# Optimization experiments

Measured on AMD Instinct MI355X. Metric: run time of the kernel, lower is better.

## Reference

```python
import jax, jax.numpy as jnp
import numpy as np

B, N, D, K = 8, 200000, 16, 512
MAX_CP = K  # upper bound on number of condensation points per event
ATTR_W, REPL_W, BG_W = 1.0, 1.0, 2.0


def setup_inputs() -> dict:
    key = jax.random.key(0)
    k1, k2, k3 = jax.random.split(key, 3)
    beta = jax.random.normal(k1, (B, N, 1), jnp.float32)
    embed = jax.random.normal(k2, (B, N, D), jnp.float32)
    r = jax.random.randint(k3, (B, N), 0, K + 8)
    slice_id = jnp.where(r < K, r, -1).astype(jnp.int32)

    def _first_occ(sid_b):
        fg = sid_b >= 0
        seg = jnp.where(fg, sid_b, K)
        fi = jax.ops.segment_min(jnp.where(fg, jnp.arange(N), N), seg, num_segments=K + 1)[:K]
        present = fi < N
        return jnp.clip(fi, 0, N - 1), present

    fi, pres = jax.vmap(_first_occ)(slice_id)
    # exactly one condensation point per present instance (its first hit)
    is_cp = jnp.zeros((B, N), jnp.int32).at[jnp.arange(B)[:, None], fi].max(pres.astype(jnp.int32))
    return {"beta": beta, "embed": embed, "slice_id": slice_id, "is_cp": is_cp}


def _per_event(beta_b, emb_b, sid, cp):
    # beta_b:[N], emb_b:[N,D], sid:[N] int, cp:[N] int
    fg = sid >= 0
    bg = ~fg
    seg = jnp.where(fg, sid, K)            # background -> dummy segment K
    sid_c = jnp.clip(sid, 0, K - 1)
    counts = jax.ops.segment_sum(fg.astype(jnp.float32), seg, num_segments=K + 1)[:K]
    present = counts > 0
    cp_fg = (cp == 1) & fg
    cp_cnt = jax.ops.segment_sum(cp_fg.astype(jnp.float32), seg, num_segments=K + 1)[:K]
    valid = present & (cp_cnt == 1)        # instances entering the CE term

    # per-instance cross-entropy: lse(beta over instance hits) - beta[cp]
    beta_m = jnp.where(fg, beta_b, -jnp.inf)
    m = jax.ops.segment_max(beta_m, seg, num_segments=K + 1)[:K]
    m_safe = jnp.where(jnp.isfinite(m), m, 0.0)
    e = jnp.where(fg, jnp.exp(beta_b - m_safe[sid_c]), 0.0)
    sumexp = jax.ops.segment_sum(e, seg, num_segments=K + 1)[:K]
    lse = m_safe + jnp.log(jnp.maximum(sumexp, 1e-30))
    cp_beta = jax.ops.segment_sum(jnp.where(cp_fg, beta_b, 0.0), seg, num_segments=K + 1)[:K]
    ce = jnp.where(valid, lse - cp_beta, 0.0)
    slice_count = jnp.sum(valid)
    beta_loss = jnp.sum(ce) / jnp.maximum(slice_count, 1)

    # background beta penalty
    nbg = jnp.sum(bg)
    bg_mean = jnp.sum(jnp.where(bg, jax.nn.sigmoid(beta_b), 0.0)) / jnp.maximum(nbg, 1)
    beta_loss = beta_loss + jnp.where(nbg > 0, BG_W * bg_mean, 0.0)

    # attraction: per instance, mean squared distance of hits to its first cp embedding
    idx = jnp.where(cp_fg, jnp.arange(N), N)
    fi = jax.ops.segment_min(idx, seg, num_segments=K + 1)[:K]
    has_cp = present & (cp_cnt >= 1)
    cp_emb = emb_b[jnp.clip(fi, 0, N - 1)]          # [K,D]
    ref = cp_emb[sid_c]                              # [N,D] gather per hit
    d = jnp.where(fg, jnp.sum((emb_b - ref) ** 2, axis=-1), 0.0)
    dsum = jax.ops.segment_sum(d, seg, num_segments=K + 1)[:K]
    attr = ATTR_W * jnp.sum(jnp.where(has_cp, dsum / jnp.maximum(counts, 1.0), 0.0))

    # repulsion: pairwise exp(-dist^2) over ALL cp hits (diagonal included, as in torch .mean())
    cp_all = cp == 1
    ncp = jnp.sum(cp_all)
    order = jnp.argsort(jnp.where(cp_all, 0, 1))     # stable: cps first, by index
    topidx = order[:MAX_CP]
    vmask = cp_all[topidx]
    ce2 = emb_b[topidx]                               # [MAX_CP, D]
    dist2 = jnp.sum((ce2[:, None, :] - ce2[None, :, :]) ** 2, axis=-1)
    w = vmask[:, None] & vmask[None, :]
    rep_sum = jnp.sum(jnp.where(w, jnp.exp(-dist2), 0.0))
    rep = jnp.where(ncp > 1, REPL_W * rep_sum / jnp.maximum(ncp * ncp, 1), 0.0)

    loss_b = beta_loss + attr + rep
    include = slice_count > 0
    return loss_b, beta_loss, attr, rep, include


def _forward(beta, embed, slice_id, is_cp):
    loss_b, bl, al, rl, inc = jax.vmap(_per_event)(beta[..., 0], embed, slice_id, is_cp)
    incf = inc.astype(loss_b.dtype)
    count = jnp.sum(incf)
    denom = jnp.maximum(count, 1.0)
    total = jnp.where(count > 0, jnp.sum(loss_b * incf) / denom, 0.0)
    beta_log = jnp.sum(bl * incf) / denom
    attr_log = jnp.sum(al * incf) / denom
    repl_log = jnp.sum(rl * incf) / denom
    return total, beta_log, attr_log, repl_log


def reference(beta, embed, slice_id, is_cp):
    return _forward(beta, embed, slice_id, is_cp)
```

## Files before the change

kernel.cpp:

```cpp
#include <hip/hip_runtime.h>
#include <math.h>

#define Bb 8
#define Nn 200000
#define Dd 16
#define Kk 512

__global__ __launch_bounds__(256) void k_init(int* packed, float* cpb, float* se,
                                              int* fi, float* ds,
                                              int* nbg, float* sig, int* cpc, float* rep) {
  int i = blockIdx.x * 256 + threadIdx.x;
  if (i < Bb * Kk) { packed[i] = 0; cpb[i] = 0.f; se[i] = 0.f; fi[i] = Nn; ds[i] = 0.f; }
  if (i < Bb) { nbg[i] = 0; sig[i] = 0.f; cpc[i] = 0; rep[i] = 0.f; }
}

__global__ __launch_bounds__(256) void k_pass1(const float* __restrict__ beta,
                                               const int* __restrict__ sid,
                                               const int* __restrict__ cp,
                                               int* packed, float* cp_beta_g, float* sumexp_g,
                                               int* fi_g, int* nbg, float* sig,
                                               int* cp_count, int* cp_idx) {
  const int b = blockIdx.y;
  __shared__ int   s_cnt[Kk];
  __shared__ float s_cb[Kk];
  __shared__ float s_se[Kk];
  __shared__ int   s_fi[Kk];
  __shared__ int   s_nbg;
  __shared__ float s_sig;
  for (int k = threadIdx.x; k < Kk; k += 256) { s_cnt[k] = 0; s_cb[k] = 0.f; s_se[k] = 0.f; s_fi[k] = Nn; }
  if (threadIdx.x == 0) { s_nbg = 0; s_sig = 0.f; }
  __syncthreads();

  const int NV = Nn / 4;
  const int nchunks = gridDim.x;
  const int chunk = (NV + nchunks - 1) / nchunks;
  const int start = blockIdx.x * chunk;
  const int end = min(start + chunk, NV);
  const size_t base = (size_t)b * Nn;
  const int4*   sid4  = (const int4*)(sid + base);
  const int4*   cp4   = (const int4*)(cp + base);
  const float4* beta4 = (const float4*)(beta + base);

  int lnbg = 0; float lsig = 0.f;
  for (int v = start + threadIdx.x; v < end; v += 256) {
    int4 s4 = sid4[v];
    int4 c4 = cp4[v];
    float4 b4 = beta4[v];
    int ss[4] = {s4.x, s4.y, s4.z, s4.w};
    int cc[4] = {c4.x, c4.y, c4.z, c4.w};
    float bb[4] = {b4.x, b4.y, b4.z, b4.w};
    #pragma unroll
    for (int t = 0; t < 4; t++) {
      int s = ss[t], c = cc[t];
      float bv = bb[t];
      int n = v * 4 + t;
      if (s >= 0) {
        atomicAdd(&s_cnt[s], 1 + ((c == 1) ? (1 << 20) : 0));
        atomicAdd(&s_se[s], __expf(bv));
        if (c == 1) {
          atomicAdd(&s_cb[s], bv);
          atomicMin(&s_fi[s], n);
        }
      } else {
        lnbg++; lsig += 1.f / (1.f + __expf(-bv));
      }
      if (c == 1) {
        int pos = atomicAdd(&cp_count[b], 1);
        if (pos < 512) cp_idx[b * 512 + pos] = n;
      }
    }
  }
  if (lnbg) { atomicAdd(&s_nbg, lnbg); atomicAdd(&s_sig, lsig); }
  __syncthreads();

  for (int k = threadIdx.x; k < Kk; k += 256) {
    int c = s_cnt[k];
    if (c) {
      atomicAdd(&packed[b * Kk + k], c);
      atomicAdd(&sumexp_g[b * Kk + k], s_se[k]);
      float cb = s_cb[k]; if (cb != 0.f) atomicAdd(&cp_beta_g[b * Kk + k], cb);
      int f = s_fi[k];    if (f < Nn)    atomicMin(&fi_g[b * Kk + k], f);
    }
  }
  if (threadIdx.x == 0 && s_nbg) { atomicAdd(&nbg[b], s_nbg); atomicAdd(&sig[b], s_sig); }
}

__global__ __launch_bounds__(256) void k_pass2(const int* __restrict__ sid,
                                               const float* __restrict__ emb,
                                               const int* __restrict__ fi_g,
                                               float* dsum_g) {
  const int b = blockIdx.y;
  __shared__ float4 s_ref4[Kk * 4];
  __shared__ float s_d[Kk];
  for (int k = threadIdx.x; k < Kk; k += 256) {
    int f = fi_g[b * Kk + k]; if (f > Nn - 1) f = Nn - 1;
    const float4* src = (const float4*)(emb + ((size_t)b * Nn + f) * Dd);
    #pragma unroll
    for (int j = 0; j < 4; j++) s_ref4[k * 4 + j] = src[j];
    s_d[k] = 0.f;
  }
  __syncthreads();

  const int NV = Nn / 4;
  const int nchunks = gridDim.x;
  const int chunk = (NV + nchunks - 1) / nchunks;
  const int start = blockIdx.x * chunk;
  const int end = min(start + chunk, NV);
  const size_t base = (size_t)b * Nn;
  const int4* sid4 = (const int4*)(sid + base);

  for (int v = start + threadIdx.x; v < end; v += 256) {
    int4 s4 = sid4[v];
    const float4* e4 = (const float4*)(emb + (base + (size_t)v * 4) * Dd);
    float4 a[16];
    #pragma unroll
    for (int t = 0; t < 16; t++) a[t] = e4[t];
    int ss[4] = {s4.x, s4.y, s4.z, s4.w};
    #pragma unroll
    for (int t = 0; t < 4; t++) {
      int s = ss[t];
      float msk = (s >= 0) ? 1.f : 0.f;
      int sc = (s < 0) ? 0 : s;
      const float4* r4 = &s_ref4[sc * 4];
      float4 r0 = r4[0], r1 = r4[1], r2 = r4[2], r3 = r4[3];
      float4 a0 = a[t*4+0], a1 = a[t*4+1], a2 = a[t*4+2], a3 = a[t*4+3];
      float d = 0.f, df;
      df = a0.x - r0.x; d = fmaf(df, df, d);
      df = a0.y - r0.y; d = fmaf(df, df, d);
      df = a0.z - r0.z; d = fmaf(df, df, d);
      df = a0.w - r0.w; d = fmaf(df, df, d);
      df = a1.x - r1.x; d = fmaf(df, df, d);
      df = a1.y - r1.y; d = fmaf(df, df, d);
      df = a1.z - r1.z; d = fmaf(df, df, d);
      df = a1.w - r1.w; d = fmaf(df, df, d);
      df = a2.x - r2.x; d = fmaf(df, df, d);
      df = a2.y - r2.y; d = fmaf(df, df, d);
      df = a2.z - r2.z; d = fmaf(df, df, d);
      df = a2.w - r2.w; d = fmaf(df, df, d);
      df = a3.x - r3.x; d = fmaf(df, df, d);
      df = a3.y - r3.y; d = fmaf(df, df, d);
      df = a3.z - r3.z; d = fmaf(df, df, d);
      df = a3.w - r3.w; d = fmaf(df, df, d);
      atomicAdd(&s_d[sc], d * msk);
    }
  }
  __syncthreads();
  for (int k = threadIdx.x; k < Kk; k += 256) {
    float v = s_d[k];
    if (v != 0.f) atomicAdd(&dsum_g[b * Kk + k], v);
  }
}

__global__ __launch_bounds__(256) void k_rep(const float* __restrict__ emb,
                                             const int* __restrict__ cp_idx,
                                             const int* __restrict__ cp_count,
                                             float* rep_acc) {
  const int b = blockIdx.y;
  int nc = cp_count[b]; if (nc > 512) nc = 512;
  __shared__ float s_e[512 * 17];
  for (int i = threadIdx.x; i < nc * 4; i += 256) {
    int r = i >> 2, j = i & 3;
    int n = cp_idx[b * 512 + r];
    float4 v = ((const float4*)(emb + ((size_t)b * Nn + n) * Dd))[j];
    s_e[r * 17 + j * 4 + 0] = v.x;
    s_e[r * 17 + j * 4 + 1] = v.y;
    s_e[r * 17 + j * 4 + 2] = v.z;
    s_e[r * 17 + j * 4 + 3] = v.w;
  }
  __syncthreads();

  const int rows = 512 / gridDim.x;
  int i = blockIdx.x * rows + (threadIdx.x >> 3);
  int js = threadIdx.x & 7;
  float acc = 0.f;
  if (i < nc) {
    float e[16];
    #pragma unroll
    for (int d = 0; d < 16; d++) e[d] = s_e[i * 17 + d];
    for (int j = js; j < nc; j += 8) {
      const float* r = &s_e[j * 17];
      float dist = 0.f;
      #pragma unroll
      for (int d = 0; d < 16; d++) { float df = e[d] - r[d]; dist += df * df; }
      acc += __expf(-dist);
    }
  }
  __shared__ float s_red;
  if (threadIdx.x == 0) s_red = 0.f;
  __syncthreads();
  for (int off = 32; off; off >>= 1) acc += __shfl_down(acc, off, 64);
  if ((threadIdx.x & 63) == 0 && acc != 0.f) atomicAdd(&s_red, acc);
  __syncthreads();
  if (threadIdx.x == 0 && s_red != 0.f) atomicAdd(&rep_acc[b], s_red);
}

__global__ __launch_bounds__(512) void k_final(const int* __restrict__ packed,
                                               const float* __restrict__ cp_beta,
                                               const float* __restrict__ sumexp,
                                               const float* __restrict__ dsum,
                                               const int* __restrict__ nbg,
                                               const float* __restrict__ sig,
                                               const int* __restrict__ cp_count,
                                               const float* __restrict__ rep_acc,
                                               float* __restrict__ out) {
  const int b = threadIdx.x >> 6;
  const int lane = threadIdx.x & 63;
  float ce = 0.f, at = 0.f, sc = 0.f;
  #pragma unroll
  for (int i = 0; i < Kk / 64; i++) {
    int k = i * 64 + lane;
    int   pc = packed[b * Kk + k];
    float se = sumexp[b * Kk + k];
    float cb = cp_beta[b * Kk + k];
    float dv = dsum[b * Kk + k];
    int cnt = pc & 0xFFFFF;
    int cpc = pc >> 20;
    if (cnt > 0) {
      if (cpc == 1) { ce += __logf(fmaxf(se, 1e-30f)) - cb; sc += 1.f; }
      if (cpc >= 1) at += dv / (float)cnt;
    }
  }
  #pragma unroll
  for (int off = 32; off; off >>= 1) {
    ce += __shfl_down(ce, off, 64);
    at += __shfl_down(at, off, 64);
    sc += __shfl_down(sc, off, 64);
  }
  __shared__ float lb_s[Bb], bl_s[Bb], al_s[Bb], rl_s[Bb];
  __shared__ int inc_s[Bb];
  if (lane == 0) {
    int scb = (int)(sc + 0.5f);
    float bl = ce / (float)max(scb, 1);
    int nb = nbg[b];
    if (nb > 0) bl += 2.0f * sig[b] / (float)nb;
    int ncp = cp_count[b];
    float rl = (ncp > 1) ? rep_acc[b] / fmaxf((float)ncp * (float)ncp, 1.f) : 0.f;
    bl_s[b] = bl; al_s[b] = at; rl_s[b] = rl; lb_s[b] = bl + at + rl;
    inc_s[b] = (scb > 0) ? 1 : 0;
  }
  __syncthreads();
  if (threadIdx.x == 0) {
    float cnt = 0.f, st = 0.f, sb = 0.f, sa = 0.f, sr = 0.f;
    for (int b2 = 0; b2 < Bb; b2++) {
      if (inc_s[b2]) { cnt += 1.f; st += lb_s[b2]; sb += bl_s[b2]; sa += al_s[b2]; sr += rl_s[b2]; }
    }
    float denom = fmaxf(cnt, 1.f);
    out[0] = (cnt > 0.f) ? st / denom : 0.f;
    out[1] = sb / denom;
    out[2] = sa / denom;
    out[3] = sr / denom;
  }
}

extern "C" void kernel_launch(void* const* d_in, const int* in_sizes, int n_in,
                              void* d_out, int out_size, void* d_ws, size_t ws_size,
                              hipStream_t stream) {
  const float* beta = (const float*)d_in[0];
  const float* emb  = (const float*)d_in[1];
  const int*   sid  = (const int*)d_in[2];
  const int*   cp   = (const int*)d_in[3];
  float* out = (float*)d_out;

  char* ws = (char*)d_ws;
  size_t off = 0;
  auto alloc = [&](size_t bytes) -> void* {
    void* p = ws + off;
    off += (bytes + 255) & ~(size_t)255;
    return p;
  };
  int*   packed   = (int*)  alloc(Bb * Kk * sizeof(int));
  float* cp_beta  = (float*)alloc(Bb * Kk * sizeof(float));
  float* sumexp   = (float*)alloc(Bb * Kk * sizeof(float));
  int*   fi       = (int*)  alloc(Bb * Kk * sizeof(int));
  float* dsum     = (float*)alloc(Bb * Kk * sizeof(float));
  int*   nbg      = (int*)  alloc(Bb * sizeof(int));
  float* sig      = (float*)alloc(Bb * sizeof(float));
  int*   cp_count = (int*)  alloc(Bb * sizeof(int));
  float* rep_acc  = (float*)alloc(Bb * sizeof(float));
  int*   cp_idx   = (int*)  alloc(Bb * 512 * sizeof(int));

  k_init<<<(Bb * Kk + 255) / 256, 256, 0, stream>>>(packed, cp_beta, sumexp, fi, dsum,
                                                    nbg, sig, cp_count, rep_acc);
  k_pass1<<<dim3(128, Bb), 256, 0, stream>>>(beta, sid, cp, packed, cp_beta, sumexp, fi,
                                             nbg, sig, cp_count, cp_idx);
  k_pass2<<<dim3(96, Bb), 256, 0, stream>>>(sid, emb, fi, dsum);
  k_rep<<<dim3(16, Bb), 256, 0, stream>>>(emb, cp_idx, cp_count, rep_acc);
  k_final<<<1, 512, 0, stream>>>(packed, cp_beta, sumexp, dsum, nbg, sig,
                                 cp_count, rep_acc, out);
}
```

Measured before the change: 218.5 us.

## Fuse distance pass and repulsion kernel into one launch with coalesced lane-split loads

Merges the per-point distance accumulation and the condensation-point repulsion kernels into a single launch, assigning 80 blocks per event to the distance work and 16 to repulsion so they run concurrently. The distance loop is restructured so four lanes cooperate on one point, each loading one float4, with shuffle reductions, giving coalesced global loads; the reference table uses a padded stride to reduce LDS bank conflicts. This removes a launch and serialization between the two stages, at the cost of extra shuffles and fewer blocks doing the bandwidth-heavy pass.

```diff
diff --git a/kernel.cpp b/kernel.cpp
--- a/kernel.cpp
+++ b/kernel.cpp
@@ -85,113 +85,114 @@
   if (threadIdx.x == 0 && s_nbg) { atomicAdd(&nbg[b], s_nbg); atomicAdd(&sig[b], s_sig); }
 }
 
-__global__ __launch_bounds__(256) void k_pass2(const int* __restrict__ sid,
-                                               const float* __restrict__ emb,
-                                               const int* __restrict__ fi_g,
-                                               float* dsum_g) {
+__global__ __launch_bounds__(256) void k_pass2rep(const int* __restrict__ sid,
+                                                  const float* __restrict__ emb,
+                                                  const int* __restrict__ fi_g,
+                                                  const int* __restrict__ cp_idx,
+                                                  const int* __restrict__ cp_count,
+                                                  float* dsum_g, float* rep_acc) {
   const int b = blockIdx.y;
-  __shared__ float4 s_ref4[Kk * 4];
+  __shared__ float4 s_ref4[Kk * 5];
   __shared__ float s_d[Kk];
-  for (int k = threadIdx.x; k < Kk; k += 256) {
-    int f = fi_g[b * Kk + k]; if (f > Nn - 1) f = Nn - 1;
-    const float4* src = (const float4*)(emb + ((size_t)b * Nn + f) * Dd);
-    #pragma unroll
-    for (int j = 0; j < 4; j++) s_ref4[k * 4 + j] = src[j];
-    s_d[k] = 0.f;
-  }
-  __syncthreads();
-
-  const int NV = Nn / 4;
-  const int nchunks = gridDim.x;
-  const int chunk = (NV + nchunks - 1) / nchunks;
-  const int start = blockIdx.x * chunk;
-  const int end = min(start + chunk, NV);
-  const size_t base = (size_t)b * Nn;
-  const int4* sid4 = (const int4*)(sid + base);
-
-  for (int v = start + threadIdx.x; v < end; v += 256) {
-    int4 s4 = sid4[v];
-    const float4* e4 = (const float4*)(emb + (base + (size_t)v * 4) * Dd);
-    float4 a[16];
-    #pragma unroll
-    for (int t = 0; t < 16; t++) a[t] = e4[t];
-    int ss[4] = {s4.x, s4.y, s4.z, s4.w};
-    #pragma unroll
-    for (int t = 0; t < 4; t++) {
-      int s = ss[t];
-      float msk = (s >= 0) ? 1.f : 0.f;
-      int sc = (s < 0) ? 0 : s;
-      const float4* r4 = &s_ref4[sc * 4];
-      float4 r0 = r4[0], r1 = r4[1], r2 = r4[2], r3 = r4[3];
-      float4 a0 = a[t*4+0], a1 = a[t*4+1], a2 = a[t*4+2], a3 = a[t*4+3];
-      float d = 0.f, df;
-      df = a0.x - r0.x; d = fmaf(df, df, d);
-      df = a0.y - r0.y; d = fmaf(df, df, d);
-      df = a0.z - r0.z; d = fmaf(df, df, d);
-      df = a0.w - r0.w; d = fmaf(df, df, d);
-      df = a1.x - r1.x; d = fmaf(df, df, d);
-      df = a1.y - r1.y; d = fmaf(df, df, d);
-      df = a1.z - r1.z; d = fmaf(df, df, d);
-      df = a1.w - r1.w; d = fmaf(df, df, d);
-      df = a2.x - r2.x; d = fmaf(df, df, d);
-      df = a2.y - r2.y; d = fmaf(df, df, d);
-      df = a2.z - r2.z; d = fmaf(df, df, d);
-      df = a2.w - r2.w; d = fmaf(df, df, d);
-      df = a3.x - r3.x; d = fmaf(df, df, d);
-      df = a3.y - r3.y; d = fmaf(df, df, d);
-      df = a3.z - r3.z; d = fmaf(df, df, d);
-      df = a3.w - r3.w; d = fmaf(df, df, d);
-      atomicAdd(&s_d[sc], d * msk);
-    }
-  }
-  __syncthreads();
-  for (int k = threadIdx.x; k < Kk; k += 256) {
-    float v = s_d[k];
-    if (v != 0.f) atomicAdd(&dsum_g[b * Kk + k], v);
-  }
-}
-
-__global__ __launch_bounds__(256) void k_rep(const float* __restrict__ emb,
-                                             const int* __restrict__ cp_idx,
-                                             const int* __restrict__ cp_count,
-                                             float* rep_acc) {
-  const int b = blockIdx.y;
-  int nc = cp_count[b]; if (nc > 512) nc = 512;
-  __shared__ float s_e[512 * 17];
-  for (int i = threadIdx.x; i < nc * 4; i += 256) {
-    int r = i >> 2, j = i & 3;
-    int n = cp_idx[b * 512 + r];
-    float4 v = ((const float4*)(emb + ((size_t)b * Nn + n) * Dd))[j];
-    s_e[r * 17 + j * 4 + 0] = v.x;
-    s_e[r * 17 + j * 4 + 1] = v.y;
-    s_e[r * 17 + j * 4 + 2] = v.z;
-    s_e[r * 17 + j * 4 + 3] = v.w;
-  }
-  __syncthreads();
-
-  const int rows = 512 / gridDim.x;
-  int i = blockIdx.x * rows + (threadIdx.x >> 3);
-  int js = threadIdx.x & 7;
-  float acc = 0.f;
-  if (i < nc) {
-    float e[16];
-    #pragma unroll
-    for (int d = 0; d < 16; d++) e[d] = s_e[i * 17 + d];
-    for (int j = js; j < nc; j += 8) {
-      const float* r = &s_e[j * 17];
-      float dist = 0.f;
+
+  if (blockIdx.x < 80) {
+    for (int k = threadIdx.x; k < Kk; k += 256) {
+      int f = fi_g[b * Kk + k]; if (f > Nn - 1) f = Nn - 1;
+      const float4* src = (const float4*)(emb + ((size_t)b * Nn + f) * Dd);
       #pragma unroll
-      for (int d = 0; d < 16; d++) { float df = e[d] - r[d]; dist += df * df; }
-      acc += __expf(-dist);
-    }
-  }
-  __shared__ float s_red;
-  if (threadIdx.x == 0) s_red = 0.f;
-  __syncthreads();
-  for (int off = 32; off; off >>= 1) acc += __shfl_down(acc, off, 64);
-  if ((threadIdx.x & 63) == 0 && acc != 0.f) atomicAdd(&s_red, acc);
-  __syncthreads();
-  if (threadIdx.x == 0 && s_red != 0.f) atomicAdd(&rep_acc[b], s_red);
+      for (int j = 0; j < 4; j++) s_ref4[k * 5 + j] = src[j];
+      s_d[k] = 0.f;
+    }
+    __syncthreads();
+
+    const int lane_j = threadIdx.x & 3;
+    const int lane_e = threadIdx.x >> 2;
+    const size_t base = (size_t)b * Nn;
+    const float4* emb4 = (const float4*)(emb + base * Dd);
+    const int g0 = blockIdx.x * 40;
+
+    #pragma unroll 2
+    for (int it = 0; it < 20; it++) {
+      int e0 = (g0 + 2 * it) * 64 + lane_e;
+      int e1 = e0 + 64;
+      int e0c = min(e0, Nn - 1), e1c = min(e1, Nn - 1);
+      int s0 = sid[base + e0c];
+      int s1 = sid[base + e1c];
+      float4 a0 = emb4[(size_t)e0c * 4 + lane_j];
+      float4 a1 = emb4[(size_t)e1c * 4 + lane_j];
+      {
+        bool ok = (e0 < Nn) && (s0 >= 0);
+        int sc = ok ? s0 : 0;
+        float4 r = s_ref4[sc * 5 + lane_j];
+        float df, d;
+        df = a0.x - r.x; d = df * df;
+        df = a0.y - r.y; d = fmaf(df, df, d);
+        df = a0.z - r.z; d = fmaf(df, df, d);
+        df = a0.w - r.w; d = fmaf(df, df, d);
+        d = ok ? d : 0.f;
+        d += __shfl_xor(d, 1, 64);
+        d += __shfl_xor(d, 2, 64);
+        if (lane_j == 0 && d != 0.f) atomicAdd(&s_d[sc], d);
+      }
+      {
+        bool ok = (e1 < Nn) && (s1 >= 0);
+        int sc = ok ? s1 : 0;
+        float4 r = s_ref4[sc * 5 + lane_j];
+        float df, d;
+        df = a1.x - r.x; d = df * df;
+        df = a1.y - r.y; d = fmaf(df, df, d);
+        df = a1.z - r.z; d = fmaf(df, df, d);
+        df = a1.w - r.w; d = fmaf(df, df, d);
+        d = ok ? d : 0.f;
+        d += __shfl_xor(d, 1, 64);
+        d += __shfl_xor(d, 2, 64);
+        if (lane_j == 0 && d != 0.f) atomicAdd(&s_d[sc], d);
+      }
+    }
+    __syncthreads();
+    for (int k = threadIdx.x; k < Kk; k += 256) {
+      float v = s_d[k];
+      if (v != 0.f) atomicAdd(&dsum_g[b * Kk + k], v);
+    }
+  } else {
+    const int bx = blockIdx.x - 80;
+    int nc = cp_count[b]; if (nc > 512) nc = 512;
+    float* s_e = (float*)s_ref4;
+    for (int i = threadIdx.x; i < nc * 4; i += 256) {
+      int r = i >> 2, j = i & 3;
+      int n = cp_idx[b * 512 + r];
+      float4 v = ((const float4*)(emb + ((size_t)b * Nn + n) * Dd))[j];
+      s_e[r * 17 + j * 4 + 0] = v.x;
+      s_e[r * 17 + j * 4 + 1] = v.y;
+      s_e[r * 17 + j * 4 + 2] = v.z;
+      s_e[r * 17 + j * 4 + 3] = v.w;
+    }
+    __syncthreads();
+
+    const int rows = 512 / 16;
+    int i = bx * rows + (threadIdx.x >> 3);
+    int js = threadIdx.x & 7;
+    float acc = 0.f;
+    if (i < nc) {
+      float e[16];
+      #pragma unroll
+      for (int d = 0; d < 16; d++) e[d] = s_e[i * 17 + d];
+      for (int j = js; j < nc; j += 8) {
+        const float* r = &s_e[j * 17];
+        float dist = 0.f;
+        #pragma unroll
+        for (int d = 0; d < 16; d++) { float df = e[d] - r[d]; dist += df * df; }
+        acc += __expf(-dist);
+      }
+    }
+    __shared__ float s_red;
+    if (threadIdx.x == 0) s_red = 0.f;
+    __syncthreads();
+    for (int off = 32; off; off >>= 1) acc += __shfl_down(acc, off, 64);
+    if ((threadIdx.x & 63) == 0 && acc != 0.f) atomicAdd(&s_red, acc);
+    __syncthreads();
+    if (threadIdx.x == 0 && s_red != 0.f) atomicAdd(&rep_acc[b], s_red);
+  }
 }
 
 __global__ __launch_bounds__(512) void k_final(const int* __restrict__ packed,
@@ -283,8 +284,7 @@
                                                     nbg, sig, cp_count, rep_acc);
   k_pass1<<<dim3(128, Bb), 256, 0, stream>>>(beta, sid, cp, packed, cp_beta, sumexp, fi,
                                              nbg, sig, cp_count, cp_idx);
-  k_pass2<<<dim3(96, Bb), 256, 0, stream>>>(sid, emb, fi, dsum);
-  k_rep<<<dim3(16, Bb), 256, 0, stream>>>(emb, cp_idx, cp_count, rep_acc);
+  k_pass2rep<<<dim3(96, Bb), 256, 0, stream>>>(sid, emb, fi, cp_idx, cp_count, dsum, rep_acc);
   k_final<<<1, 512, 0, stream>>>(packed, cp_beta, sumexp, dsum, nbg, sig,
                                  cp_count, rep_acc, out);
 }
```

Result: faster. 204.7 us (-6.3%).
